# Kernel tuning notes

Hardware: AMD Instinct MI355X
Metric: run time of the kernel (lower is better)

Reference implementation:

```python
import jax, jax.numpy as jnp
import numpy as np

B, K, D, DK, DG, H = 4, 512, 768, 96, 96, 8  # batch, proposals, appearance, key, geo, n_relations


def setup_inputs() -> dict:
    key = jax.random.key(0)
    ks = jax.random.split(key, 12)
    s = 0.02
    return {
        "f_a": jax.random.normal(ks[0], (B, K, D), dtype=jnp.float32),
        "position_embedding": jax.random.uniform(ks[1], (B, K, K, DG), dtype=jnp.float32),
        "WG_w": jax.random.normal(ks[2], (H, DG), dtype=jnp.float32) * s,
        "WG_b": jnp.zeros((H,), dtype=jnp.float32),
        "WK_w": jax.random.normal(ks[3], (H, D, DK), dtype=jnp.float32) * s,
        "WK_b": jnp.zeros((H, DK), dtype=jnp.float32),
        "WQ_w": jax.random.normal(ks[4], (H, D, DK), dtype=jnp.float32) * s,
        "WQ_b": jnp.zeros((H, DK), dtype=jnp.float32),
        "WV_w": jax.random.normal(ks[5], (H, D, DK), dtype=jnp.float32) * s,
        "WV_b": jnp.zeros((H, DK), dtype=jnp.float32),
        "gamma": jnp.asarray(0.5, dtype=jnp.float32),
    }


def reference(f_a, position_embedding, WG_w, WG_b, WK_w, WK_b, WQ_w, WQ_b, WV_w, WV_b, gamma):
    dim_k = WK_w.shape[-1]
    # per-head projections: (B,K,D) x (H,D,DK) -> (B,H,K,DK)
    w_k = jnp.einsum('bkd,hdf->bhkf', f_a, WK_w) + WK_b[None, :, None, :]
    w_q = jnp.einsum('bkd,hdf->bhkf', f_a, WQ_w) + WQ_b[None, :, None, :]
    w_v = jnp.einsum('bkd,hdf->bhkf', f_a, WV_w) + WV_b[None, :, None, :]
    # scaled_dot[b,h,i,j] = <w_k[b,h,i], w_q[b,h,j]> / sqrt(dim_k)  (i: key row, j: query col)
    scores = jnp.einsum('bhif,bhjf->bhij', w_k, w_q) / np.sqrt(dim_k)
    # geometric gate: WG is Linear(DG, 1) per head, then ReLU -> (B,H,K,K)
    w_g = jax.nn.relu(jnp.einsum('bijg,hg->bhij', position_embedding, WG_w)
                      + WG_b[None, :, None, None])
    logits = jnp.log(jnp.clip(w_g, 1e-6, None)) + scores
    # torch Softmax(dim=1) over (B,K,K) = over the key index i -> axis 2 here
    attn = jax.nn.softmax(logits, axis=2)
    # output[b,j] = sum_i attn[b,h,i,j] * w_v[b,h,i,:]  -> (B,K,H,DK)
    out = jnp.einsum('bhij,bhif->bjhf', attn, w_v)
    b, k = f_a.shape[:2]
    concat = out.reshape(b, k, -1)  # concat over Nr heads, last dim = H*DK = D
    return gamma * concat + f_a
```

## Files before the change

kernel.cpp:

```cpp
#include <hip/hip_runtime.h>
#include <hip/hip_bf16.h>

#define B_ 4
#define K_ 512
#define D_ 768
#define DK_ 96
#define DG_ 96
#define H_ 8

typedef __attribute__((ext_vector_type(8))) __bf16 bf16x8;
typedef __attribute__((ext_vector_type(4))) float f32x4;

static __device__ __forceinline__ unsigned short f2bf(float x) {
  union { float f; unsigned int u; } v; v.f = x;
  unsigned int u = v.u;
  return (unsigned short)((u + 0x7FFFu + ((u >> 16) & 1u)) >> 16);
}

__global__ __launch_bounds__(256) void cast_fa_kernel(const float* __restrict__ fa,
                                                      unsigned short* __restrict__ fa16) {
  int t = blockIdx.x * 256 + threadIdx.x;
  float4 v = ((const float4*)fa)[t];
  ushort4 o;
  o.x = f2bf(v.x); o.y = f2bf(v.y); o.z = f2bf(v.z); o.w = f2bf(v.w);
  ((ushort4*)fa16)[t] = o;
}

__global__ __launch_bounds__(256) void prep_w_kernel(const float* __restrict__ wq,
                                                     const float* __restrict__ wk,
                                                     const float* __restrict__ wv,
                                                     unsigned short* __restrict__ wt16) {
  __shared__ unsigned short Ts[96][130];
  int bid = blockIdx.x;
  int dt = bid % 6; int rest = bid / 6;
  int h = rest % 8; int p = rest / 8;
  const float* w = (p == 0) ? wq : (p == 1) ? wk : wv;
  const float* src = w + ((size_t)h * D_ + dt * 128) * DK_;
  for (int c = threadIdx.x; c < 128 * 96; c += 256) {
    int dd = c / 96, f = c % 96;
    Ts[f][dd] = f2bf(src[c]);
  }
  __syncthreads();
  unsigned short* dst = wt16 + (size_t)(p * H_ + h) * DK_ * D_ + dt * 128;
  for (int c = threadIdx.x; c < 96 * 32; c += 256) {
    int f = c / 32, q = c % 32;
    ushort4 v;
    v.x = Ts[f][q * 4 + 0]; v.y = Ts[f][q * 4 + 1];
    v.z = Ts[f][q * 4 + 2]; v.w = Ts[f][q * 4 + 3];
    *(ushort4*)(dst + (size_t)f * D_ + q * 4) = v;
  }
}

__global__ __launch_bounds__(256) void proj_kernel(
    const unsigned short* __restrict__ fa16, const unsigned short* __restrict__ wt16,
    const float* __restrict__ bq, const float* __restrict__ bk, const float* __restrict__ bv,
    unsigned short* __restrict__ q16, unsigned short* __restrict__ k16,
    unsigned short* __restrict__ v16) {
  int bid = blockIdx.x;
  int mt = bid & 3;  bid >>= 2;
  int b  = bid & 3;  bid >>= 2;
  int h  = bid & 7;  bid >>= 3;
  int p  = bid;
  int lane = threadIdx.x & 63, wid = threadIdx.x >> 6;
  int lr = lane & 15, lg = lane >> 4;
  int row0 = mt * 128 + wid * 32;

  const unsigned short* A  = fa16 + ((size_t)(b * K_ + row0)) * D_;
  const unsigned short* Bt = wt16 + ((size_t)(p * H_ + h)) * DK_ * D_;

  f32x4 acc[2][6];
#pragma unroll
  for (int i = 0; i < 2; i++)
#pragma unroll
    for (int c = 0; c < 6; c++) acc[i][c] = (f32x4){0.f, 0.f, 0.f, 0.f};

  for (int kk = 0; kk < D_ / 32; kk++) {
    bf16x8 a0 = *(const bf16x8*)(A + (size_t)(0 * 16 + lr) * D_ + kk * 32 + lg * 8);
    bf16x8 a1 = *(const bf16x8*)(A + (size_t)(1 * 16 + lr) * D_ + kk * 32 + lg * 8);
#pragma unroll
    for (int c = 0; c < 6; c++) {
      bf16x8 bfr = *(const bf16x8*)(Bt + (size_t)(c * 16 + lr) * D_ + kk * 32 + lg * 8);
      acc[0][c] = __builtin_amdgcn_mfma_f32_16x16x32_bf16(a0, bfr, acc[0][c], 0, 0, 0);
      acc[1][c] = __builtin_amdgcn_mfma_f32_16x16x32_bf16(a1, bfr, acc[1][c], 0, 0, 0);
    }
  }

  const float* bias = (p == 0) ? bq : (p == 1) ? bk : bv;
  unsigned short* dst = (p == 0) ? q16 : (p == 1) ? k16 : v16;
#pragma unroll
  for (int i = 0; i < 2; i++) {
#pragma unroll
    for (int c = 0; c < 6; c++) {
      int col = c * 16 + lr;
      float bb = bias[h * DK_ + col];
#pragma unroll
      for (int r = 0; r < 4; r++) {
        int row = row0 + i * 16 + lg * 4 + r;
        float val = acc[i][c][r] + bb;
        dst[((size_t)(b * H_ + h) * K_ + row) * DK_ + col] = f2bf(val);
      }
    }
  }
}

__global__ __launch_bounds__(256) void vtrans_kernel(const unsigned short* __restrict__ v16,
                                                     unsigned short* __restrict__ vt16) {
  __shared__ unsigned short Ts[96][130];
  int bid = blockIdx.x;
  int it = bid & 3; int bh = bid >> 2;
  const unsigned short* src = v16 + ((size_t)bh * K_ + it * 128) * DK_;
  for (int c = threadIdx.x; c < 128 * 96 / 4; c += 256) {
    int flat = c * 4;
    int ii = flat / 96, f = flat % 96;
    ushort4 v = *(const ushort4*)(src + flat);
    Ts[f + 0][ii] = v.x; Ts[f + 1][ii] = v.y; Ts[f + 2][ii] = v.z; Ts[f + 3][ii] = v.w;
  }
  __syncthreads();
  unsigned short* dst = vt16 + (size_t)bh * DK_ * K_ + it * 128;
  for (int c = threadIdx.x; c < 96 * 32; c += 256) {
    int f = c / 32, q = c % 32;
    ushort4 v;
    v.x = Ts[f][q * 4 + 0]; v.y = Ts[f][q * 4 + 1];
    v.z = Ts[f][q * 4 + 2]; v.w = Ts[f][q * 4 + 3];
    *(ushort4*)(dst + (size_t)f * K_ + q * 4) = v;
  }
}

__global__ __launch_bounds__(256) void scores_kernel(const unsigned short* __restrict__ q16,
                                                     const unsigned short* __restrict__ k16,
                                                     float* __restrict__ L) {
  int bid = blockIdx.x;
  int it = bid & 3;  bid >>= 2;
  int jt = bid & 3;  bid >>= 2;
  int h  = bid & 7;  bid >>= 3;
  int b  = bid;
  int lane = threadIdx.x & 63, wid = threadIdx.x >> 6;
  int lr = lane & 15, lg = lane >> 4;
  int j0 = jt * 128 + wid * 32;
  int i0 = it * 128;
  const unsigned short* Q  = q16 + ((size_t)(b * H_ + h) * K_ + j0) * DK_;
  const unsigned short* Kp = k16 + ((size_t)(b * H_ + h) * K_ + i0) * DK_;

  f32x4 acc[2][8];
#pragma unroll
  for (int x = 0; x < 2; x++)
#pragma unroll
    for (int c = 0; c < 8; c++) acc[x][c] = (f32x4){0.f, 0.f, 0.f, 0.f};

#pragma unroll
  for (int kk = 0; kk < 3; kk++) {
    bf16x8 a0 = *(const bf16x8*)(Q + (size_t)lr * DK_ + kk * 32 + lg * 8);
    bf16x8 a1 = *(const bf16x8*)(Q + (size_t)(16 + lr) * DK_ + kk * 32 + lg * 8);
#pragma unroll
    for (int c = 0; c < 8; c++) {
      bf16x8 bfr = *(const bf16x8*)(Kp + (size_t)(c * 16 + lr) * DK_ + kk * 32 + lg * 8);
      acc[0][c] = __builtin_amdgcn_mfma_f32_16x16x32_bf16(a0, bfr, acc[0][c], 0, 0, 0);
      acc[1][c] = __builtin_amdgcn_mfma_f32_16x16x32_bf16(a1, bfr, acc[1][c], 0, 0, 0);
    }
  }

  const float scale = 0.10206207261596577f;
  float* Lb = L + ((size_t)(b * H_ + h) * K_ + j0) * K_ + i0;
#pragma unroll
  for (int x = 0; x < 2; x++)
#pragma unroll
    for (int c = 0; c < 8; c++)
#pragma unroll
      for (int r = 0; r < 4; r++) {
        int jl = x * 16 + lg * 4 + r;
        int il = c * 16 + lr;
        Lb[(size_t)jl * K_ + il] = acc[x][c][r] * scale;
      }
}

#define GS_PAD 516
__global__ __launch_bounds__(512) void gatesm_kernel(
    const float* __restrict__ pe, const float* __restrict__ wgw,
    const float* __restrict__ wgb, const float* __restrict__ L,
    unsigned short* __restrict__ p16) {
  extern __shared__ float Ls[];
  int b = blockIdx.x >> 7;
  int j0 = (blockIdx.x & 127) * 4;
  int t = threadIdx.x;
  int wv = t >> 6, lane = t & 63;
  int lr3 = (lane >> 3) & 7;
  int lg3 = lane & 7;
  const float4* pe4 = (const float4*)pe;
  const float4* wg4 = (const float4*)wgw;

  for (int p = 0; p < 8; p++) {
    int i = wv * 64 + p * 8 + lr3;
    float4 pev[4][3];
#pragma unroll
    for (int j = 0; j < 4; j++) {
      size_t base = ((size_t)(b * K_ + i) * K_ + (j0 + j)) * (DG_ / 4);
#pragma unroll
      for (int c = 0; c < 3; c++) pev[j][c] = pe4[base + lg3 + 8 * c];
    }
#pragma unroll
    for (int h = 0; h < H_; h++) {
      float4 w0 = wg4[h * 24 + lg3];
      float4 w1 = wg4[h * 24 + lg3 + 8];
      float4 w2 = wg4[h * 24 + lg3 + 16];
      float bias = wgb[h];
      float acc[4];
#pragma unroll
      for (int j = 0; j < 4; j++) {
        acc[j] = pev[j][0].x * w0.x + pev[j][0].y * w0.y + pev[j][0].z * w0.z + pev[j][0].w * w0.w
               + pev[j][1].x * w1.x + pev[j][1].y * w1.y + pev[j][1].z * w1.z + pev[j][1].w * w1.w
               + pev[j][2].x * w2.x + pev[j][2].y * w2.y + pev[j][2].z * w2.z + pev[j][2].w * w2.w;
      }
#pragma unroll
      for (int j = 0; j < 4; j++) {
        acc[j] += __shfl_xor(acc[j], 1);
        acc[j] += __shfl_xor(acc[j], 2);
        acc[j] += __shfl_xor(acc[j], 4);
      }
      if (lg3 == h) {
#pragma unroll
        for (int j = 0; j < 4; j++) {
          float lgt = __logf(fmaxf(acc[j] + bias, 1e-6f));
          Ls[(h * 4 + j) * GS_PAD + i] = lgt;
        }
      }
    }
  }
  __syncthreads();

#pragma unroll
  for (int rr = 0; rr < 4; rr++) {
    int row = wv * 4 + rr;
    int h = row >> 2, j = row & 3;
    const float* Lr = &Ls[row * GS_PAD];
    const float* Lg = L + ((size_t)(b * H_ + h) * K_ + (j0 + j)) * K_;
    float4 g0 = *(const float4*)(Lr + lane * 4);
    float4 g1 = *(const float4*)(Lr + 256 + lane * 4);
    float4 s0 = *(const float4*)(Lg + lane * 4);
    float4 s1 = *(const float4*)(Lg + 256 + lane * 4);
    float l0 = g0.x + s0.x, l1 = g0.y + s0.y, l2 = g0.z + s0.z, l3 = g0.w + s0.w;
    float l4 = g1.x + s1.x, l5 = g1.y + s1.y, l6 = g1.z + s1.z, l7 = g1.w + s1.w;
    float m = fmaxf(fmaxf(fmaxf(l0, l1), fmaxf(l2, l3)),
                    fmaxf(fmaxf(l4, l5), fmaxf(l6, l7)));
#pragma unroll
    for (int o = 32; o > 0; o >>= 1) m = fmaxf(m, __shfl_xor(m, o));
    float e0 = __expf(l0 - m), e1 = __expf(l1 - m), e2 = __expf(l2 - m), e3 = __expf(l3 - m);
    float e4 = __expf(l4 - m), e5 = __expf(l5 - m), e6 = __expf(l6 - m), e7 = __expf(l7 - m);
    float s = ((e0 + e1) + (e2 + e3)) + ((e4 + e5) + (e6 + e7));
#pragma unroll
    for (int o = 32; o > 0; o >>= 1) s += __shfl_xor(s, o);
    float inv = 1.0f / s;
    ushort4 o0, o1;
    o0.x = f2bf(e0 * inv); o0.y = f2bf(e1 * inv); o0.z = f2bf(e2 * inv); o0.w = f2bf(e3 * inv);
    o1.x = f2bf(e4 * inv); o1.y = f2bf(e5 * inv); o1.z = f2bf(e6 * inv); o1.w = f2bf(e7 * inv);
    ushort4* dst = (ushort4*)(p16 + ((size_t)(b * H_ + h) * K_ + (j0 + j)) * K_);
    dst[lane] = o0;
    dst[lane + 64] = o1;
  }
}

__global__ __launch_bounds__(256) void pv_kernel(const unsigned short* __restrict__ p16,
                                                 const unsigned short* __restrict__ vt16,
                                                 const float* __restrict__ fa,
                                                 const float* __restrict__ gptr,
                                                 float* __restrict__ out) {
  int bid = blockIdx.x;
  int mt = bid & 7; bid >>= 3;
  int h  = bid & 7; bid >>= 3;
  int b  = bid;
  int lane = threadIdx.x & 63, wid = threadIdx.x >> 6;
  int lr = lane & 15, lg = lane >> 4;
  int bh = b * H_ + h;
  int row0 = mt * 64 + wid * 16;
  const unsigned short* A = p16 + ((size_t)bh * K_ + row0) * K_;
  const unsigned short* V = vt16 + (size_t)bh * DK_ * K_;

  f32x4 acc[6];
#pragma unroll
  for (int c = 0; c < 6; c++) acc[c] = (f32x4){0.f, 0.f, 0.f, 0.f};

  for (int kk = 0; kk < 16; kk++) {
    bf16x8 a = *(const bf16x8*)(A + (size_t)lr * K_ + kk * 32 + lg * 8);
#pragma unroll
    for (int c = 0; c < 6; c++) {
      bf16x8 bfr = *(const bf16x8*)(V + (size_t)(c * 16 + lr) * K_ + kk * 32 + lg * 8);
      acc[c] = __builtin_amdgcn_mfma_f32_16x16x32_bf16(a, bfr, acc[c], 0, 0, 0);
    }
  }

  float gamma = gptr[0];
#pragma unroll
  for (int c = 0; c < 6; c++) {
    int fcol = c * 16 + lr;
#pragma unroll
    for (int r = 0; r < 4; r++) {
      int j = row0 + lg * 4 + r;
      size_t oidx = ((size_t)(b * K_ + j)) * D_ + h * DK_ + fcol;
      out[oidx] = gamma * acc[c][r] + fa[oidx];
    }
  }
}

extern "C" void kernel_launch(void* const* d_in, const int* in_sizes, int n_in,
                              void* d_out, int out_size, void* d_ws, size_t ws_size,
                              hipStream_t stream) {
  (void)in_sizes; (void)n_in; (void)out_size; (void)ws_size;
  const float* fa   = (const float*)d_in[0];
  const float* pe   = (const float*)d_in[1];
  const float* wgw  = (const float*)d_in[2];
  const float* wgb  = (const float*)d_in[3];
  const float* wkw  = (const float*)d_in[4];
  const float* wkb  = (const float*)d_in[5];
  const float* wqw  = (const float*)d_in[6];
  const float* wqb  = (const float*)d_in[7];
  const float* wvw  = (const float*)d_in[8];
  const float* wvb  = (const float*)d_in[9];
  const float* gptr = (const float*)d_in[10];
  float* out = (float*)d_out;

  char* ws = (char*)d_ws;
  unsigned short* fa16 = (unsigned short*)ws; ws += (size_t)B_ * K_ * D_ * 2;
  unsigned short* wt16 = (unsigned short*)ws; ws += (size_t)3 * H_ * DK_ * D_ * 2;
  unsigned short* q16  = (unsigned short*)ws; ws += (size_t)B_ * H_ * K_ * DK_ * 2;
  unsigned short* k16  = (unsigned short*)ws; ws += (size_t)B_ * H_ * K_ * DK_ * 2;
  unsigned short* v16  = (unsigned short*)ws; ws += (size_t)B_ * H_ * K_ * DK_ * 2;
  unsigned short* vt16 = (unsigned short*)ws; ws += (size_t)B_ * H_ * DK_ * K_ * 2;
  float* L             = (float*)ws;          ws += (size_t)B_ * H_ * K_ * K_ * 4;
  unsigned short* p16  = (unsigned short*)ws;

  const int lds_bytes = 32 * GS_PAD * 4;
  hipFuncSetAttribute((const void*)gatesm_kernel,
                      hipFuncAttributeMaxDynamicSharedMemorySize, lds_bytes);

  cast_fa_kernel<<<(B_ * K_ * D_ / 4) / 256, 256, 0, stream>>>(fa, fa16);
  prep_w_kernel<<<144, 256, 0, stream>>>(wqw, wkw, wvw, wt16);
  proj_kernel<<<3 * H_ * B_ * 4, 256, 0, stream>>>(fa16, wt16, wqb, wkb, wvb, q16, k16, v16);
  vtrans_kernel<<<128, 256, 0, stream>>>(v16, vt16);
  scores_kernel<<<B_ * H_ * 4 * 4, 256, 0, stream>>>(q16, k16, L);
  gatesm_kernel<<<B_ * 128, 512, lds_bytes, stream>>>(pe, wgw, wgb, L, p16);
  pv_kernel<<<B_ * H_ * 8, 256, 0, stream>>>(p16, vt16, fa, gptr, out);
}
```

Measured before the change: 192.4 us.

## Merge independent prep and vtrans/scores kernels, shrink projection tiles for more blocks

Combines the fa cast and weight-transpose kernels into one launch, and the V-transpose and scores kernels into another, using block-index ranges to pick the branch. This removes two kernel launches and lets independent work overlap within one grid. The projection kernel now has each wave compute a 16-row tile instead of 32 rows, doubling the grid to 768 blocks for better CU occupancy. The cost is that each loaded weight fragment is reused across fewer rows, which adds redundant B loads.

New measurement: 197.7 us. 1.03x slower.

```diff
diff --git a/kernel.cpp b/kernel.cpp
--- a/kernel.cpp
+++ b/kernel.cpp
@@ -17,37 +17,38 @@
   return (unsigned short)((u + 0x7FFFu + ((u >> 16) & 1u)) >> 16);
 }
 
-__global__ __launch_bounds__(256) void cast_fa_kernel(const float* __restrict__ fa,
-                                                      unsigned short* __restrict__ fa16) {
-  int t = blockIdx.x * 256 + threadIdx.x;
-  float4 v = ((const float4*)fa)[t];
-  ushort4 o;
-  o.x = f2bf(v.x); o.y = f2bf(v.y); o.z = f2bf(v.z); o.w = f2bf(v.w);
-  ((ushort4*)fa16)[t] = o;
-}
-
-__global__ __launch_bounds__(256) void prep_w_kernel(const float* __restrict__ wq,
-                                                     const float* __restrict__ wk,
-                                                     const float* __restrict__ wv,
-                                                     unsigned short* __restrict__ wt16) {
+__global__ __launch_bounds__(256) void prep_kernel(const float* __restrict__ fa,
+                                                   unsigned short* __restrict__ fa16,
+                                                   const float* __restrict__ wq,
+                                                   const float* __restrict__ wk,
+                                                   const float* __restrict__ wv,
+                                                   unsigned short* __restrict__ wt16) {
   __shared__ unsigned short Ts[96][130];
-  int bid = blockIdx.x;
-  int dt = bid % 6; int rest = bid / 6;
-  int h = rest % 8; int p = rest / 8;
-  const float* w = (p == 0) ? wq : (p == 1) ? wk : wv;
-  const float* src = w + ((size_t)h * D_ + dt * 128) * DK_;
-  for (int c = threadIdx.x; c < 128 * 96; c += 256) {
-    int dd = c / 96, f = c % 96;
-    Ts[f][dd] = f2bf(src[c]);
-  }
-  __syncthreads();
-  unsigned short* dst = wt16 + (size_t)(p * H_ + h) * DK_ * D_ + dt * 128;
-  for (int c = threadIdx.x; c < 96 * 32; c += 256) {
-    int f = c / 32, q = c % 32;
-    ushort4 v;
-    v.x = Ts[f][q * 4 + 0]; v.y = Ts[f][q * 4 + 1];
-    v.z = Ts[f][q * 4 + 2]; v.w = Ts[f][q * 4 + 3];
-    *(ushort4*)(dst + (size_t)f * D_ + q * 4) = v;
+  if (blockIdx.x < 1536) {
+    int t = blockIdx.x * 256 + threadIdx.x;
+    float4 v = ((const float4*)fa)[t];
+    ushort4 o;
+    o.x = f2bf(v.x); o.y = f2bf(v.y); o.z = f2bf(v.z); o.w = f2bf(v.w);
+    ((ushort4*)fa16)[t] = o;
+  } else {
+    int bid = blockIdx.x - 1536;
+    int dt = bid % 6; int rest = bid / 6;
+    int h = rest % 8; int p = rest / 8;
+    const float* w = (p == 0) ? wq : (p == 1) ? wk : wv;
+    const float* src = w + ((size_t)h * D_ + dt * 128) * DK_;
+    for (int c = threadIdx.x; c < 128 * 96; c += 256) {
+      int dd = c / 96, f = c % 96;
+      Ts[f][dd] = f2bf(src[c]);
+    }
+    __syncthreads();
+    unsigned short* dst = wt16 + (size_t)(p * H_ + h) * DK_ * D_ + dt * 128;
+    for (int c = threadIdx.x; c < 96 * 32; c += 256) {
+      int f = c / 32, q = c % 32;
+      ushort4 v;
+      v.x = Ts[f][q * 4 + 0]; v.y = Ts[f][q * 4 + 1];
+      v.z = Ts[f][q * 4 + 2]; v.w = Ts[f][q * 4 + 3];
+      *(ushort4*)(dst + (size_t)f * D_ + q * 4) = v;
+    }
   }
 }
 
@@ -57,120 +58,114 @@
     unsigned short* __restrict__ q16, unsigned short* __restrict__ k16,
     unsigned short* __restrict__ v16) {
   int bid = blockIdx.x;
-  int mt = bid & 3;  bid >>= 2;
+  int mt = bid & 7;  bid >>= 3;
   int b  = bid & 3;  bid >>= 2;
   int h  = bid & 7;  bid >>= 3;
   int p  = bid;
   int lane = threadIdx.x & 63, wid = threadIdx.x >> 6;
   int lr = lane & 15, lg = lane >> 4;
-  int row0 = mt * 128 + wid * 32;
+  int row0 = mt * 64 + wid * 16;
 
   const unsigned short* A  = fa16 + ((size_t)(b * K_ + row0)) * D_;
   const unsigned short* Bt = wt16 + ((size_t)(p * H_ + h)) * DK_ * D_;
 
-  f32x4 acc[2][6];
-#pragma unroll
-  for (int i = 0; i < 2; i++)
-#pragma unroll
-    for (int c = 0; c < 6; c++) acc[i][c] = (f32x4){0.f, 0.f, 0.f, 0.f};
+  f32x4 acc[6];
+#pragma unroll
+  for (int c = 0; c < 6; c++) acc[c] = (f32x4){0.f, 0.f, 0.f, 0.f};
 
   for (int kk = 0; kk < D_ / 32; kk++) {
-    bf16x8 a0 = *(const bf16x8*)(A + (size_t)(0 * 16 + lr) * D_ + kk * 32 + lg * 8);
-    bf16x8 a1 = *(const bf16x8*)(A + (size_t)(1 * 16 + lr) * D_ + kk * 32 + lg * 8);
+    bf16x8 a = *(const bf16x8*)(A + (size_t)lr * D_ + kk * 32 + lg * 8);
 #pragma unroll
     for (int c = 0; c < 6; c++) {
       bf16x8 bfr = *(const bf16x8*)(Bt + (size_t)(c * 16 + lr) * D_ + kk * 32 + lg * 8);
-      acc[0][c] = __builtin_amdgcn_mfma_f32_16x16x32_bf16(a0, bfr, acc[0][c], 0, 0, 0);
-      acc[1][c] = __builtin_amdgcn_mfma_f32_16x16x32_bf16(a1, bfr, acc[1][c], 0, 0, 0);
+      acc[c] = __builtin_amdgcn_mfma_f32_16x16x32_bf16(a, bfr, acc[c], 0, 0, 0);
     }
   }
 
   const float* bias = (p == 0) ? bq : (p == 1) ? bk : bv;
   unsigned short* dst = (p == 0) ? q16 : (p == 1) ? k16 : v16;
 #pragma unroll
-  for (int i = 0; i < 2; i++) {
-#pragma unroll
-    for (int c = 0; c < 6; c++) {
-      int col = c * 16 + lr;
-      float bb = bias[h * DK_ + col];
-#pragma unroll
-      for (int r = 0; r < 4; r++) {
-        int row = row0 + i * 16 + lg * 4 + r;
-        float val = acc[i][c][r] + bb;
-        dst[((size_t)(b * H_ + h) * K_ + row) * DK_ + col] = f2bf(val);
+  for (int c = 0; c < 6; c++) {
+    int col = c * 16 + lr;
+    float bb = bias[h * DK_ + col];
+#pragma unroll
+    for (int r = 0; r < 4; r++) {
+      int row = row0 + lg * 4 + r;
+      float val = acc[c][r] + bb;
+      dst[((size_t)(b * H_ + h) * K_ + row) * DK_ + col] = f2bf(val);
+    }
+  }
+}
+
+__global__ __launch_bounds__(256) void vtscores_kernel(const unsigned short* __restrict__ q16,
+                                                       const unsigned short* __restrict__ k16,
+                                                       float* __restrict__ L,
+                                                       const unsigned short* __restrict__ v16,
+                                                       unsigned short* __restrict__ vt16) {
+  __shared__ unsigned short Ts[96][130];
+  if (blockIdx.x < 512) {
+    int bid = blockIdx.x;
+    int it = bid & 3;  bid >>= 2;
+    int jt = bid & 3;  bid >>= 2;
+    int h  = bid & 7;  bid >>= 3;
+    int b  = bid;
+    int lane = threadIdx.x & 63, wid = threadIdx.x >> 6;
+    int lr = lane & 15, lg = lane >> 4;
+    int j0 = jt * 128 + wid * 32;
+    int i0 = it * 128;
+    const unsigned short* Q  = q16 + ((size_t)(b * H_ + h) * K_ + j0) * DK_;
+    const unsigned short* Kp = k16 + ((size_t)(b * H_ + h) * K_ + i0) * DK_;
+
+    f32x4 acc[2][8];
+#pragma unroll
+    for (int x = 0; x < 2; x++)
+#pragma unroll
+      for (int c = 0; c < 8; c++) acc[x][c] = (f32x4){0.f, 0.f, 0.f, 0.f};
+
+#pragma unroll
+    for (int kk = 0; kk < 3; kk++) {
+      bf16x8 a0 = *(const bf16x8*)(Q + (size_t)lr * DK_ + kk * 32 + lg * 8);
+      bf16x8 a1 = *(const bf16x8*)(Q + (size_t)(16 + lr) * DK_ + kk * 32 + lg * 8);
+#pragma unroll
+      for (int c = 0; c < 8; c++) {
+        bf16x8 bfr = *(const bf16x8*)(Kp + (size_t)(c * 16 + lr) * DK_ + kk * 32 + lg * 8);
+        acc[0][c] = __builtin_amdgcn_mfma_f32_16x16x32_bf16(a0, bfr, acc[0][c], 0, 0, 0);
+        acc[1][c] = __builtin_amdgcn_mfma_f32_16x16x32_bf16(a1, bfr, acc[1][c], 0, 0, 0);
       }
     }
-  }
-}
-
-__global__ __launch_bounds__(256) void vtrans_kernel(const unsigned short* __restrict__ v16,
-                                                     unsigned short* __restrict__ vt16) {
-  __shared__ unsigned short Ts[96][130];
-  int bid = blockIdx.x;
-  int it = bid & 3; int bh = bid >> 2;
-  const unsigned short* src = v16 + ((size_t)bh * K_ + it * 128) * DK_;
-  for (int c = threadIdx.x; c < 128 * 96 / 4; c += 256) {
-    int flat = c * 4;
-    int ii = flat / 96, f = flat % 96;
-    ushort4 v = *(const ushort4*)(src + flat);
-    Ts[f + 0][ii] = v.x; Ts[f + 1][ii] = v.y; Ts[f + 2][ii] = v.z; Ts[f + 3][ii] = v.w;
-  }
-  __syncthreads();
-  unsigned short* dst = vt16 + (size_t)bh * DK_ * K_ + it * 128;
-  for (int c = threadIdx.x; c < 96 * 32; c += 256) {
-    int f = c / 32, q = c % 32;
-    ushort4 v;
-    v.x = Ts[f][q * 4 + 0]; v.y = Ts[f][q * 4 + 1];
-    v.z = Ts[f][q * 4 + 2]; v.w = Ts[f][q * 4 + 3];
-    *(ushort4*)(dst + (size_t)f * K_ + q * 4) = v;
-  }
-}
-
-__global__ __launch_bounds__(256) void scores_kernel(const unsigned short* __restrict__ q16,
-                                                     const unsigned short* __restrict__ k16,
-                                                     float* __restrict__ L) {
-  int bid = blockIdx.x;
-  int it = bid & 3;  bid >>= 2;
-  int jt = bid & 3;  bid >>= 2;
-  int h  = bid & 7;  bid >>= 3;
-  int b  = bid;
-  int lane = threadIdx.x & 63, wid = threadIdx.x >> 6;
-  int lr = lane & 15, lg = lane >> 4;
-  int j0 = jt * 128 + wid * 32;
-  int i0 = it * 128;
-  const unsigned short* Q  = q16 + ((size_t)(b * H_ + h) * K_ + j0) * DK_;
-  const unsigned short* Kp = k16 + ((size_t)(b * H_ + h) * K_ + i0) * DK_;
-
-  f32x4 acc[2][8];
-#pragma unroll
-  for (int x = 0; x < 2; x++)
-#pragma unroll
-    for (int c = 0; c < 8; c++) acc[x][c] = (f32x4){0.f, 0.f, 0.f, 0.f};
-
-#pragma unroll
-  for (int kk = 0; kk < 3; kk++) {
-    bf16x8 a0 = *(const bf16x8*)(Q + (size_t)lr * DK_ + kk * 32 + lg * 8);
-    bf16x8 a1 = *(const bf16x8*)(Q + (size_t)(16 + lr) * DK_ + kk * 32 + lg * 8);
-#pragma unroll
-    for (int c = 0; c < 8; c++) {
-      bf16x8 bfr = *(const bf16x8*)(Kp + (size_t)(c * 16 + lr) * DK_ + kk * 32 + lg * 8);
-      acc[0][c] = __builtin_amdgcn_mfma_f32_16x16x32_bf16(a0, bfr, acc[0][c], 0, 0, 0);
-      acc[1][c] = __builtin_amdgcn_mfma_f32_16x16x32_bf16(a1, bfr, acc[1][c], 0, 0, 0);
-    }
-  }
-
-  const float scale = 0.10206207261596577f;
-  float* Lb = L + ((size_t)(b * H_ + h) * K_ + j0) * K_ + i0;
-#pragma unroll
-  for (int x = 0; x < 2; x++)
-#pragma unroll
-    for (int c = 0; c < 8; c++)
-#pragma unroll
-      for (int r = 0; r < 4; r++) {
-        int jl = x * 16 + lg * 4 + r;
-        int il = c * 16 + lr;
-        Lb[(size_t)jl * K_ + il] = acc[x][c][r] * scale;
-      }
+
+    const float scale = 0.10206207261596577f;
+    float* Lb = L + ((size_t)(b * H_ + h) * K_ + j0) * K_ + i0;
+#pragma unroll
+    for (int x = 0; x < 2; x++)
+#pragma unroll
+      for (int c = 0; c < 8; c++)
+#pragma unroll
+        for (int r = 0; r < 4; r++) {
+          int jl = x * 16 + lg * 4 + r;
+          int il = c * 16 + lr;
+          Lb[(size_t)jl * K_ + il] = acc[x][c][r] * scale;
+        }
+  } else {
+    int bid = blockIdx.x - 512;
+    int it = bid & 3; int bh = bid >> 2;
+    const unsigned short* src = v16 + ((size_t)bh * K_ + it * 128) * DK_;
+    for (int c = threadIdx.x; c < 128 * 96 / 4; c += 256) {
+      int flat = c * 4;
+      int ii = flat / 96, f = flat % 96;
+      ushort4 v = *(const ushort4*)(src + flat);
+      Ts[f + 0][ii] = v.x; Ts[f + 1][ii] = v.y; Ts[f + 2][ii] = v.z; Ts[f + 3][ii] = v.w;
+    }
+    __syncthreads();
+    unsigned short* dst = vt16 + (size_t)bh * DK_ * K_ + it * 128;
+    for (int c = threadIdx.x; c < 96 * 32; c += 256) {
+      int f = c / 32, q = c % 32;
+      ushort4 v;
+      v.x = Ts[f][q * 4 + 0]; v.y = Ts[f][q * 4 + 1];
+      v.z = Ts[f][q * 4 + 2]; v.w = Ts[f][q * 4 + 3];
+      *(ushort4*)(dst + (size_t)f * K_ + q * 4) = v;
+    }
+  }
 }
 
 #define GS_PAD 516
@@ -331,11 +326,9 @@
   hipFuncSetAttribute((const void*)gatesm_kernel,
                       hipFuncAttributeMaxDynamicSharedMemorySize, lds_bytes);
 
-  cast_fa_kernel<<<(B_ * K_ * D_ / 4) / 256, 256, 0, stream>>>(fa, fa16);
-  prep_w_kernel<<<144, 256, 0, stream>>>(wqw, wkw, wvw, wt16);
-  proj_kernel<<<3 * H_ * B_ * 4, 256, 0, stream>>>(fa16, wt16, wqb, wkb, wvb, q16, k16, v16);
-  vtrans_kernel<<<128, 256, 0, stream>>>(v16, vt16);
-  scores_kernel<<<B_ * H_ * 4 * 4, 256, 0, stream>>>(q16, k16, L);
+  prep_kernel<<<1536 + 144, 256, 0, stream>>>(fa, fa16, wqw, wkw, wvw, wt16);
+  proj_kernel<<<768, 256, 0, stream>>>(fa16, wt16, wqb, wkb, wvb, q16, k16, v16);
+  vtscores_kernel<<<512 + 128, 256, 0, stream>>>(q16, k16, L, v16, vt16);
   gatesm_kernel<<<B_ * 128, 512, lds_bytes, stream>>>(pe, wgw, wgb, L, p16);
   pv_kernel<<<B_ * H_ * 8, 256, 0, stream>>>(p16, vt16, fa, gptr, out);
 }
```

## Fuse V transpose into projection epilogue and double-buffer projection loads

Applied to the files above, without the earlier changes.

The projection kernel now writes the V projection already transposed, staging it through shared memory in its epilogue. This removes the separate vtrans kernel launch and the round trip of V through global memory. The main MFMA loop is also software-pipelined with two register sets, so the next k-slice's A and B fragments load while the current one computes. The cost is higher register pressure and shared memory use in every projection block.

Result: faster. 186.2 us (-3.2%).

```diff
diff --git a/kernel.cpp b/kernel.cpp
--- a/kernel.cpp
+++ b/kernel.cpp
@@ -55,7 +55,8 @@
     const unsigned short* __restrict__ fa16, const unsigned short* __restrict__ wt16,
     const float* __restrict__ bq, const float* __restrict__ bk, const float* __restrict__ bv,
     unsigned short* __restrict__ q16, unsigned short* __restrict__ k16,
-    unsigned short* __restrict__ v16) {
+    unsigned short* __restrict__ vt16) {
+  __shared__ unsigned short Ts[96][130];
   int bid = blockIdx.x;
   int mt = bid & 3;  bid >>= 2;
   int b  = bid & 3;  bid >>= 2;
@@ -74,55 +75,67 @@
 #pragma unroll
     for (int c = 0; c < 6; c++) acc[i][c] = (f32x4){0.f, 0.f, 0.f, 0.f};
 
-  for (int kk = 0; kk < D_ / 32; kk++) {
-    bf16x8 a0 = *(const bf16x8*)(A + (size_t)(0 * 16 + lr) * D_ + kk * 32 + lg * 8);
-    bf16x8 a1 = *(const bf16x8*)(A + (size_t)(1 * 16 + lr) * D_ + kk * 32 + lg * 8);
+  auto LOADF = [&](bf16x8& a0, bf16x8& a1, bf16x8 (&bb)[6], int kk) {
+    a0 = *(const bf16x8*)(A + (size_t)lr * D_ + kk * 32 + lg * 8);
+    a1 = *(const bf16x8*)(A + (size_t)(16 + lr) * D_ + kk * 32 + lg * 8);
+#pragma unroll
+    for (int c = 0; c < 6; c++)
+      bb[c] = *(const bf16x8*)(Bt + (size_t)(c * 16 + lr) * D_ + kk * 32 + lg * 8);
+  };
+  auto MF = [&](bf16x8& a0, bf16x8& a1, bf16x8 (&bb)[6]) {
 #pragma unroll
     for (int c = 0; c < 6; c++) {
-      bf16x8 bfr = *(const bf16x8*)(Bt + (size_t)(c * 16 + lr) * D_ + kk * 32 + lg * 8);
-      acc[0][c] = __builtin_amdgcn_mfma_f32_16x16x32_bf16(a0, bfr, acc[0][c], 0, 0, 0);
-      acc[1][c] = __builtin_amdgcn_mfma_f32_16x16x32_bf16(a1, bfr, acc[1][c], 0, 0, 0);
-    }
+      acc[0][c] = __builtin_amdgcn_mfma_f32_16x16x32_bf16(a0, bb[c], acc[0][c], 0, 0, 0);
+      acc[1][c] = __builtin_amdgcn_mfma_f32_16x16x32_bf16(a1, bb[c], acc[1][c], 0, 0, 0);
+    }
+  };
+
+  bf16x8 a0X, a1X, bX[6], a0Y, a1Y, bY[6];
+  LOADF(a0X, a1X, bX, 0);
+  for (int kk = 0; kk < 24; kk += 2) {
+    LOADF(a0Y, a1Y, bY, kk + 1);
+    MF(a0X, a1X, bX);
+    if (kk + 2 < 24) LOADF(a0X, a1X, bX, kk + 2);
+    MF(a0Y, a1Y, bY);
   }
 
   const float* bias = (p == 0) ? bq : (p == 1) ? bk : bv;
-  unsigned short* dst = (p == 0) ? q16 : (p == 1) ? k16 : v16;
-#pragma unroll
-  for (int i = 0; i < 2; i++) {
-#pragma unroll
-    for (int c = 0; c < 6; c++) {
-      int col = c * 16 + lr;
-      float bb = bias[h * DK_ + col];
-#pragma unroll
-      for (int r = 0; r < 4; r++) {
-        int row = row0 + i * 16 + lg * 4 + r;
-        float val = acc[i][c][r] + bb;
-        dst[((size_t)(b * H_ + h) * K_ + row) * DK_ + col] = f2bf(val);
-      }
-    }
-  }
-}
-
-__global__ __launch_bounds__(256) void vtrans_kernel(const unsigned short* __restrict__ v16,
-                                                     unsigned short* __restrict__ vt16) {
-  __shared__ unsigned short Ts[96][130];
-  int bid = blockIdx.x;
-  int it = bid & 3; int bh = bid >> 2;
-  const unsigned short* src = v16 + ((size_t)bh * K_ + it * 128) * DK_;
-  for (int c = threadIdx.x; c < 128 * 96 / 4; c += 256) {
-    int flat = c * 4;
-    int ii = flat / 96, f = flat % 96;
-    ushort4 v = *(const ushort4*)(src + flat);
-    Ts[f + 0][ii] = v.x; Ts[f + 1][ii] = v.y; Ts[f + 2][ii] = v.z; Ts[f + 3][ii] = v.w;
-  }
-  __syncthreads();
-  unsigned short* dst = vt16 + (size_t)bh * DK_ * K_ + it * 128;
-  for (int c = threadIdx.x; c < 96 * 32; c += 256) {
-    int f = c / 32, q = c % 32;
-    ushort4 v;
-    v.x = Ts[f][q * 4 + 0]; v.y = Ts[f][q * 4 + 1];
-    v.z = Ts[f][q * 4 + 2]; v.w = Ts[f][q * 4 + 3];
-    *(ushort4*)(dst + (size_t)f * K_ + q * 4) = v;
+  if (p == 2) {
+#pragma unroll
+    for (int i = 0; i < 2; i++)
+#pragma unroll
+      for (int c = 0; c < 6; c++) {
+        int col = c * 16 + lr;
+        float bb = bias[h * DK_ + col];
+#pragma unroll
+        for (int r = 0; r < 4; r++) {
+          int lrow = wid * 32 + i * 16 + lg * 4 + r;
+          Ts[col][lrow] = f2bf(acc[i][c][r] + bb);
+        }
+      }
+    __syncthreads();
+    unsigned short* dst = vt16 + (size_t)(b * H_ + h) * DK_ * K_ + mt * 128;
+    for (int c2 = threadIdx.x; c2 < 96 * 32; c2 += 256) {
+      int f = c2 / 32, q = c2 % 32;
+      ushort4 v;
+      v.x = Ts[f][q * 4 + 0]; v.y = Ts[f][q * 4 + 1];
+      v.z = Ts[f][q * 4 + 2]; v.w = Ts[f][q * 4 + 3];
+      *(ushort4*)(dst + (size_t)f * K_ + q * 4) = v;
+    }
+  } else {
+    unsigned short* dst = (p == 0) ? q16 : k16;
+#pragma unroll
+    for (int i = 0; i < 2; i++)
+#pragma unroll
+      for (int c = 0; c < 6; c++) {
+        int col = c * 16 + lr;
+        float bb = bias[h * DK_ + col];
+#pragma unroll
+        for (int r = 0; r < 4; r++) {
+          int row = row0 + i * 16 + lg * 4 + r;
+          dst[((size_t)(b * H_ + h) * K_ + row) * DK_ + col] = f2bf(acc[i][c][r] + bb);
+        }
+      }
   }
 }
 
@@ -322,7 +335,6 @@
   unsigned short* wt16 = (unsigned short*)ws; ws += (size_t)3 * H_ * DK_ * D_ * 2;
   unsigned short* q16  = (unsigned short*)ws; ws += (size_t)B_ * H_ * K_ * DK_ * 2;
   unsigned short* k16  = (unsigned short*)ws; ws += (size_t)B_ * H_ * K_ * DK_ * 2;
-  unsigned short* v16  = (unsigned short*)ws; ws += (size_t)B_ * H_ * K_ * DK_ * 2;
   unsigned short* vt16 = (unsigned short*)ws; ws += (size_t)B_ * H_ * DK_ * K_ * 2;
   float* L             = (float*)ws;          ws += (size_t)B_ * H_ * K_ * K_ * 4;
   unsigned short* p16  = (unsigned short*)ws;
@@ -333,8 +345,7 @@
 
   cast_fa_kernel<<<(B_ * K_ * D_ / 4) / 256, 256, 0, stream>>>(fa, fa16);
   prep_w_kernel<<<144, 256, 0, stream>>>(wqw, wkw, wvw, wt16);
-  proj_kernel<<<3 * H_ * B_ * 4, 256, 0, stream>>>(fa16, wt16, wqb, wkb, wvb, q16, k16, v16);
-  vtrans_kernel<<<128, 256, 0, stream>>>(v16, vt16);
+  proj_kernel<<<3 * H_ * B_ * 4, 256, 0, stream>>>(fa16, wt16, wqb, wkb, wvb, q16, k16, vt16);
   scores_kernel<<<B_ * H_ * 4 * 4, 256, 0, stream>>>(q16, k16, L);
   gatesm_kernel<<<B_ * 128, 512, lds_bytes, stream>>>(pe, wgw, wgb, L, p16);
   pv_kernel<<<B_ * H_ * 8, 256, 0, stream>>>(p16, vt16, fa, gptr, out);
```
